# Kernel tuning notes

Measured on AMD Instinct MI355X. Metric: run time of the kernel, lower is better.

The kernel has to match this reference:

```python
import jax, jax.numpy as jnp
import numpy as np

H = 256; W = 256; TS = 4
EYE_Z = 2.732                     # nr camera position (0,0,2.732)
FOCAL = float(1.0 / np.tan(np.deg2rad(15.0)))  # 30-deg viewing angle
BIG = 1e10
EPS = 1e-8


def _render(vertices, faces, textures, angle):
    """Differentiable z-buffer rasterizer with trilinear per-face texture cubes.
    Ambient light = 1.0, directional = 0.0, so shading == sampled texture color."""
    v = vertices[0]                    # [V,3]
    f = faces[0]                       # [F,3] int
    tex = jnp.tanh(textures)[0]        # [F,TS,TS,TS,3]
    P = H * W

    # camera orbit: rotate mesh about y by angle (fraction of full turn)
    th = angle[0] * (2.0 * jnp.pi)
    c, s = jnp.cos(th), jnp.sin(th)
    x, y, z = v[:, 0], v[:, 1], v[:, 2]
    xr = c * x + s * z
    zr = -s * x + c * z
    depth = EYE_Z - zr                 # camera at (0,0,EYE_Z) looking down -z
    px = FOCAL * xr / depth
    py = FOCAL * y / depth

    fx = px[f]; fy = py[f]; fd = depth[f]      # [F,3]
    ax, bx, cx = fx[:, 0], fx[:, 1], fx[:, 2]
    ay, by, cy = fy[:, 0], fy[:, 1], fy[:, 2]

    # pixel centers in NDC [-1,1]
    xs = (jnp.arange(W) + 0.5) / W * 2.0 - 1.0
    ys = 1.0 - (jnp.arange(H) + 0.5) / H * 2.0
    gy, gx = jnp.meshgrid(ys, xs, indexing='ij')
    pxp = gx.reshape(-1)[:, None]      # [P,1]
    pyp = gy.reshape(-1)[:, None]

    area = (bx - ax) * (cy - ay) - (by - ay) * (cx - ax)
    valid = jnp.abs(area) > EPS
    denom = jnp.where(valid, area, 1.0)

    def edge(x0, y0, x1, y1):
        # normalized edge function -> barycentric weight, shape [P,F]
        return ((x1 - x0) * (pyp - y0) - (y1 - y0) * (pxp - x0)) / denom

    w0 = edge(bx, by, cx, cy)
    w1 = edge(cx, cy, ax, ay)
    w2 = 1.0 - w0 - w1
    inside = (w0 >= 0) & (w1 >= 0) & (w2 >= 0) & valid[None, :]

    zpix = w0 * fd[:, 0] + w1 * fd[:, 1] + w2 * fd[:, 2]   # interpolated depth
    zbuf = jnp.where(inside & (zpix > EPS), zpix, BIG)
    fidx = jnp.argmin(zbuf, axis=1)                        # [P] winning face
    hit = jnp.take_along_axis(zbuf, fidx[:, None], 1)[:, 0] < 0.5 * BIG

    w0s = jnp.take_along_axis(w0, fidx[:, None], 1)[:, 0]
    w1s = jnp.take_along_axis(w1, fidx[:, None], 1)[:, 0]
    pw = jnp.stack([w0s, w1s, 1.0 - w0s - w1s], axis=-1)   # [P,3] barycentric

    # trilinear sample of the per-face TSxTSxTS texture cube at barycentric coords
    u = jnp.clip(pw, 0.0, 1.0) * (TS - 1)
    i0 = jnp.clip(jnp.floor(u), 0, TS - 2).astype(jnp.int32)
    fr = u - i0
    texp = tex[fidx].reshape(P, TS * TS * TS, 3)           # [P,64,3]
    col = jnp.zeros((P, 3), dtype=textures.dtype)
    for a in (0, 1):
        for b in (0, 1):
            for cc in (0, 1):
                idxf = (i0[:, 0] + a) * TS * TS + (i0[:, 1] + b) * TS + (i0[:, 2] + cc)
                wc = (jnp.where(a, fr[:, 0], 1.0 - fr[:, 0])
                      * jnp.where(b, fr[:, 1], 1.0 - fr[:, 1])
                      * jnp.where(cc, fr[:, 2], 1.0 - fr[:, 2]))
                col = col + wc[:, None] * jnp.take_along_axis(texp, idxf[:, None, None], axis=1)[:, 0, :]
    col = jnp.where(hit[:, None], col, 0.0)                # black background
    return col.T.reshape(1, 3, H, W)


def setup_inputs():
    key = jax.random.key(0)
    k1, k2, k3, k4, k5 = jax.random.split(key, 5)
    V, F = 322, 640
    vertices = 0.4 * jax.random.normal(k1, (1, V, 3), dtype=jnp.float32)
    faces = jax.random.randint(k2, (1, F, 3), 0, V, dtype=jnp.int32)
    textures = 0.5 * jax.random.normal(k3, (1, F, TS, TS, TS, 3), dtype=jnp.float32)
    image_ref = jax.random.uniform(k4, (1, 3, H, W), dtype=jnp.float32)
    angle = jax.random.uniform(k5, (1,), dtype=jnp.float32)
    return {"vertices": vertices, "faces": faces, "textures": textures,
            "image_ref": image_ref, "angle": angle}


def reference(vertices, faces, textures, image_ref, angle):
    image = _render(vertices, faces, textures, angle)
    return jnp.sum((image - image_ref) ** 2)
```

## Files before the change

kernel.cpp:

```cpp
#include <hip/hip_runtime.h>
#include <math.h>

#define NH 256
#define NW 256
#define NP (NH*NW)
#define NF 640
#define NBLK 512
#define EYE_Z 2.732f
#define BIGF 1.0e10f
#define EPSF 1.0e-8f
#define FOCALF 3.7320508075688776f


__global__ __launch_bounds__(256, 2) void fused_kernel(
    const float* __restrict__ vertices,
    const int* __restrict__ faces,
    const float* __restrict__ textures,
    const float* __restrict__ angle,
    const float* __restrict__ ref,
    float* __restrict__ partials)
{
    __shared__ float4 sf[NF * 3];
    __shared__ float candZ[4][128];
    __shared__ int   candF[4][128];
    __shared__ float psum[2];

    int tid = threadIdx.x;
    int wave = tid >> 6;
    int lane = tid & 63;

    float th = angle[0] * 6.283185307179586f;
    float cth = cosf(th), sth = sinf(th);
    for (int j = tid; j < NF; j += 256) {
        float vx[3], vy[3], vd[3];
#pragma unroll
        for (int k = 0; k < 3; k++) {
            int vi = faces[j * 3 + k];
            float x = vertices[vi * 3 + 0];
            float y = vertices[vi * 3 + 1];
            float z = vertices[vi * 3 + 2];
            float xr = cth * x + sth * z;
            float zr = -sth * x + cth * z;
            float depth = EYE_Z - zr;
            vx[k] = FOCALF * xr / depth;
            vy[k] = FOCALF * y / depth;
            vd[k] = depth;
        }
        float ax = vx[0], ay = vy[0], bx = vx[1], by = vy[1], cx = vx[2], cy = vy[2];
        float area = (bx - ax) * (cy - ay) - (by - ay) * (cx - ax);
        float4 d0, d1, d2;
        if (fabsf(area) > EPSF) {
            float inv = 1.0f / area;
            float A0 = -(cy - by) * inv;
            float B0 = (cx - bx) * inv;
            float C0 = (bx * (cy - by) - by * (cx - bx)) * inv;
            float A1 = -(ay - cy) * inv;
            float B1 = (ax - cx) * inv;
            float C1 = (cx * (ay - cy) - cy * (ax - cx)) * inv;
            float zA = vd[0] - vd[2];
            float zB = vd[1] - vd[2];
            float Az = zA * A0 + zB * A1;
            float Bz = zA * B0 + zB * B1;
            float Cz = zA * C0 + zB * C1 + vd[2];
            d0 = make_float4(A0, B0, C0, A1);
            d1 = make_float4(B1, C1, Az, Bz);
            d2 = make_float4(Cz, 0.f, 0.f, 0.f);
        } else {
            d0 = make_float4(0.f, 0.f, -1.f, 0.f);
            d1 = make_float4(0.f, 0.f, 0.f, 0.f);
            d2 = make_float4(0.f, 0.f, 0.f, 0.f);
        }
        sf[j * 3 + 0] = d0;
        sf[j * 3 + 1] = d1;
        sf[j * 3 + 2] = d2;
    }
    __syncthreads();

    int base = blockIdx.x * 128;
    int row = base >> 8;
    int col0 = (base & 255) + lane;
    float px0 = ((float)col0 + 0.5f) * (1.0f / 128.0f) - 1.0f;
    float py = 1.0f - ((float)row + 0.5f) * (1.0f / 128.0f);

    float zmin0 = BIGF, zmin1 = BIGF;
    int best0 = wave * 160, best1 = wave * 160;
    int fbeg = wave * 160;
#pragma unroll 4
    for (int k = 0; k < 160; ++k) {
        int f = fbeg + k;
        float4 d0 = sf[f * 3 + 0];
        float4 d1 = sf[f * 3 + 1];
        float zC = sf[f * 3 + 2].x;
        float w0a = fmaf(d0.x, px0, fmaf(d0.y, py, d0.z));
        float w1a = fmaf(d0.w, px0, fmaf(d1.x, py, d1.y));
        float za  = fmaf(d1.z, px0, fmaf(d1.w, py, zC));
        float w0b = fmaf(0.5f, d0.x, w0a);
        float w1b = fmaf(0.5f, d0.w, w1a);
        float zb  = fmaf(0.5f, d1.z, za);
        float w2a = 1.f - w0a - w1a;
        float w2b = 1.f - w0b - w1b;
        float mna = fminf(fminf(w0a, w1a), w2a);
        float mnb = fminf(fminf(w0b, w1b), w2b);
        bool oka = (mna >= 0.f) && (za > EPSF) && (za < zmin0);
        bool okb = (mnb >= 0.f) && (zb > EPSF) && (zb < zmin1);
        zmin0 = oka ? za : zmin0;
        best0 = oka ? f : best0;
        zmin1 = okb ? zb : zmin1;
        best1 = okb ? f : best1;
    }
    candZ[wave][lane] = zmin0;
    candZ[wave][64 + lane] = zmin1;
    candF[wave][lane] = best0;
    candF[wave][64 + lane] = best1;
    __syncthreads();

    if (wave < 2) {
        int q = wave * 64 + lane;
        float zb = candZ[0][q];
        int fb = candF[0][q];
#pragma unroll
        for (int k = 1; k < 4; ++k) {
            float zk = candZ[k][q];
            int fk = candF[k][q];
            bool t = zk < zb;
            zb = t ? zk : zb;
            fb = t ? fk : fb;
        }
        bool hit = zb < 0.5f * BIGF;

        int p = base + q;
        float pxq = ((float)((base & 255) + q) + 0.5f) * (1.0f / 128.0f) - 1.0f;
        float4 d0 = sf[fb * 3 + 0];
        float4 d1 = sf[fb * 3 + 1];
        float bw0 = fmaf(d0.x, pxq, fmaf(d0.y, py, d0.z));
        float bw1 = fmaf(d0.w, pxq, fmaf(d1.x, py, d1.y));
        float pw2 = 1.f - bw0 - bw1;
        float u0 = fminf(fmaxf(bw0, 0.f), 1.f) * 3.f;
        float u1 = fminf(fmaxf(bw1, 0.f), 1.f) * 3.f;
        float u2 = fminf(fmaxf(pw2, 0.f), 1.f) * 3.f;
        int i0 = min(max((int)floorf(u0), 0), 2);
        int i1 = min(max((int)floorf(u1), 0), 2);
        int i2 = min(max((int)floorf(u2), 0), 2);
        float fr0 = u0 - (float)i0;
        float fr1 = u1 - (float)i1;
        float fr2 = u2 - (float)i2;

        const float* tb = textures + fb * 192;
        float cr = 0.f, cg = 0.f, cb = 0.f;
#pragma unroll
        for (int a = 0; a < 2; a++) {
#pragma unroll
            for (int bbi = 0; bbi < 2; bbi++) {
#pragma unroll
                for (int cc = 0; cc < 2; cc++) {
                    int idx = ((i0 + a) * 16 + (i1 + bbi) * 4 + (i2 + cc)) * 3;
                    float w = (a ? fr0 : 1.f - fr0) * (bbi ? fr1 : 1.f - fr1) * (cc ? fr2 : 1.f - fr2);
                    cr = fmaf(w, tanhf(tb[idx + 0]), cr);
                    cg = fmaf(w, tanhf(tb[idx + 1]), cg);
                    cb = fmaf(w, tanhf(tb[idx + 2]), cb);
                }
            }
        }
        if (!hit) { cr = 0.f; cg = 0.f; cb = 0.f; }

        float e0 = cr - ref[p];
        float e1 = cg - ref[NP + p];
        float e2 = cb - ref[2 * NP + p];
        float e = fmaf(e0, e0, fmaf(e1, e1, e2 * e2));
#pragma unroll
        for (int off = 32; off > 0; off >>= 1) e += __shfl_down(e, off, 64);
        if (lane == 0) psum[wave] = e;
    }
    __syncthreads();
    if (tid == 0) partials[blockIdx.x] = psum[0] + psum[1];
}

__global__ __launch_bounds__(256) void reduce_kernel(
    const float* __restrict__ partials, float* __restrict__ out)
{
    __shared__ float wsum[4];
    int tid = threadIdx.x;
    float s = partials[tid] + partials[tid + 256];
#pragma unroll
    for (int off = 32; off > 0; off >>= 1) s += __shfl_down(s, off, 64);
    int lane = tid & 63;
    int wid = tid >> 6;
    if (lane == 0) wsum[wid] = s;
    __syncthreads();
    if (tid == 0) out[0] = wsum[0] + wsum[1] + wsum[2] + wsum[3];
}

extern "C" void kernel_launch(void* const* d_in, const int* in_sizes, int n_in,
                              void* d_out, int out_size, void* d_ws, size_t ws_size,
                              hipStream_t stream) {
    const float* vertices = (const float*)d_in[0];
    const int* faces = (const int*)d_in[1];
    const float* textures = (const float*)d_in[2];
    const float* image_ref = (const float*)d_in[3];
    const float* angle = (const float*)d_in[4];
    float* out = (float*)d_out;
    float* partials = (float*)d_ws;

    fused_kernel<<<NBLK, 256, 0, stream>>>(vertices, faces, textures, angle,
                                           image_ref, partials);
    reduce_kernel<<<1, 256, 0, stream>>>(partials, out);
}
```

Baseline: 86.60 us.

## Tile-based face culling per block with compacted face lists and pretransformed textures

Each block now covers a 16x8 pixel tile and builds a compacted list of only the faces whose bounding box and edge functions overlap the tile, using ballot/popcount stream compaction in shared memory. The per-pixel depth test then loops over the culled list instead of all 640 faces. Vertices are projected once into shared memory instead of once per face corner. A separate prep kernel applies tanh to the textures once and pads them into float4 entries so each texel is fetched with one vector load. The change adds an extra kernel launch and several block barriers. The reduced face count per tile depends on the triangle sizes in the mesh.

Measured after the change: 75.67 us. 12.6% less time.

```diff
diff --git a/kernel.cpp b/kernel.cpp
--- a/kernel.cpp
+++ b/kernel.cpp
@@ -4,23 +4,43 @@
 #define NH 256
 #define NW 256
 #define NP (NH*NW)
+#define NV 322
 #define NF 640
-#define NBLK 512
 #define EYE_Z 2.732f
 #define BIGF 1.0e10f
 #define EPSF 1.0e-8f
 #define FOCALF 3.7320508075688776f
-
+#define TILE_W 16
+#define TILE_H 8
+#define NTX (NW/TILE_W)
+#define NTY (NH/TILE_H)
+#define NBLK (NTX*NTY)
+#define CULL_PAD 1e-5f
+
+
+__global__ void texprep_kernel(const float* __restrict__ textures,
+                               float4* __restrict__ texPad)
+{
+    int e = blockIdx.x * 256 + threadIdx.x;
+    float v = tanhf(textures[e]);
+    int fidx = e / 192;
+    int r = e - fidx * 192;
+    int t = r / 3;
+    int ch = r - t * 3;
+    ((float*)&texPad[fidx * 64 + t])[ch] = v;
+}
 
 __global__ __launch_bounds__(256, 2) void fused_kernel(
     const float* __restrict__ vertices,
     const int* __restrict__ faces,
-    const float* __restrict__ textures,
     const float* __restrict__ angle,
+    const float4* __restrict__ texPad,
     const float* __restrict__ ref,
     float* __restrict__ partials)
 {
-    __shared__ float4 sf[NF * 3];
+    __shared__ float4 pv[NV];
+    __shared__ float4 list[NF * 3];
+    __shared__ int wcnt[4];
     __shared__ float candZ[4][128];
     __shared__ int   candF[4][128];
     __shared__ float psum[2];
@@ -31,109 +51,140 @@
 
     float th = angle[0] * 6.283185307179586f;
     float cth = cosf(th), sth = sinf(th);
-    for (int j = tid; j < NF; j += 256) {
-        float vx[3], vy[3], vd[3];
-#pragma unroll
-        for (int k = 0; k < 3; k++) {
-            int vi = faces[j * 3 + k];
-            float x = vertices[vi * 3 + 0];
-            float y = vertices[vi * 3 + 1];
-            float z = vertices[vi * 3 + 2];
-            float xr = cth * x + sth * z;
-            float zr = -sth * x + cth * z;
-            float depth = EYE_Z - zr;
-            vx[k] = FOCALF * xr / depth;
-            vy[k] = FOCALF * y / depth;
-            vd[k] = depth;
-        }
-        float ax = vx[0], ay = vy[0], bx = vx[1], by = vy[1], cx = vx[2], cy = vy[2];
-        float area = (bx - ax) * (cy - ay) - (by - ay) * (cx - ax);
-        float4 d0, d1, d2;
-        if (fabsf(area) > EPSF) {
-            float inv = 1.0f / area;
-            float A0 = -(cy - by) * inv;
-            float B0 = (cx - bx) * inv;
-            float C0 = (bx * (cy - by) - by * (cx - bx)) * inv;
-            float A1 = -(ay - cy) * inv;
-            float B1 = (ax - cx) * inv;
-            float C1 = (cx * (ay - cy) - cy * (ax - cx)) * inv;
-            float zA = vd[0] - vd[2];
-            float zB = vd[1] - vd[2];
-            float Az = zA * A0 + zB * A1;
-            float Bz = zA * B0 + zB * B1;
-            float Cz = zA * C0 + zB * C1 + vd[2];
-            d0 = make_float4(A0, B0, C0, A1);
-            d1 = make_float4(B1, C1, Az, Bz);
-            d2 = make_float4(Cz, 0.f, 0.f, 0.f);
-        } else {
-            d0 = make_float4(0.f, 0.f, -1.f, 0.f);
-            d1 = make_float4(0.f, 0.f, 0.f, 0.f);
-            d2 = make_float4(0.f, 0.f, 0.f, 0.f);
-        }
-        sf[j * 3 + 0] = d0;
-        sf[j * 3 + 1] = d1;
-        sf[j * 3 + 2] = d2;
-    }
-    __syncthreads();
-
-    int base = blockIdx.x * 128;
-    int row = base >> 8;
-    int col0 = (base & 255) + lane;
-    float px0 = ((float)col0 + 0.5f) * (1.0f / 128.0f) - 1.0f;
-    float py = 1.0f - ((float)row + 0.5f) * (1.0f / 128.0f);
+    for (int t = tid; t < NV; t += 256) {
+        float x = vertices[t * 3 + 0];
+        float y = vertices[t * 3 + 1];
+        float z = vertices[t * 3 + 2];
+        float xr = cth * x + sth * z;
+        float zr = -sth * x + cth * z;
+        float depth = EYE_Z - zr;
+        pv[t] = make_float4(FOCALF * xr / depth, FOCALF * y / depth, depth, 0.f);
+    }
+    __syncthreads();
+
+    int tc = blockIdx.x & (NTX - 1);
+    int tr = blockIdx.x >> 4;
+    float x0 = ((float)(tc * TILE_W) + 0.5f) * (1.f / 128.f) - 1.f;
+    float x1 = ((float)(tc * TILE_W + TILE_W - 1) + 0.5f) * (1.f / 128.f) - 1.f;
+    float y1 = 1.f - ((float)(tr * TILE_H) + 0.5f) * (1.f / 128.f);
+    float y0 = 1.f - ((float)(tr * TILE_H + TILE_H - 1) + 0.5f) * (1.f / 128.f);
+
+    int nfl = 0;
+    for (int rd = 0; rd < 3; ++rd) {
+        int f = rd * 256 + tid;
+        bool accept = false;
+        float4 e0, e1, e2;
+        if (f < NF) {
+            int i0 = faces[f * 3 + 0], i1 = faces[f * 3 + 1], i2 = faces[f * 3 + 2];
+            float4 pa = pv[i0], pb = pv[i1], pc = pv[i2];
+            float area = (pb.x - pa.x) * (pc.y - pa.y) - (pb.y - pa.y) * (pc.x - pa.x);
+            if (fabsf(area) > EPSF) {
+                float xmn = fminf(fminf(pa.x, pb.x), pc.x);
+                float xmx = fmaxf(fmaxf(pa.x, pb.x), pc.x);
+                float ymn = fminf(fminf(pa.y, pb.y), pc.y);
+                float ymx = fmaxf(fmaxf(pa.y, pb.y), pc.y);
+                if (xmx >= x0 - CULL_PAD && xmn <= x1 + CULL_PAD &&
+                    ymx >= y0 - CULL_PAD && ymn <= y1 + CULL_PAD) {
+                    float inv = 1.0f / area;
+                    float A0 = -(pc.y - pb.y) * inv;
+                    float B0 =  (pc.x - pb.x) * inv;
+                    float C0 =  (pb.x * (pc.y - pb.y) - pb.y * (pc.x - pb.x)) * inv;
+                    float A1 = -(pa.y - pc.y) * inv;
+                    float B1 =  (pa.x - pc.x) * inv;
+                    float C1 =  (pc.x * (pa.y - pc.y) - pc.y * (pa.x - pc.x)) * inv;
+                    float A2 = -(A0 + A1), B2 = -(B0 + B1), C2 = 1.f - C0 - C1;
+                    float m0 = C0 + fmaxf(A0 * x0, A0 * x1) + fmaxf(B0 * y0, B0 * y1);
+                    float m1 = C1 + fmaxf(A1 * x0, A1 * x1) + fmaxf(B1 * y0, B1 * y1);
+                    float m2 = C2 + fmaxf(A2 * x0, A2 * x1) + fmaxf(B2 * y0, B2 * y1);
+                    if (m0 >= -CULL_PAD && m1 >= -CULL_PAD && m2 >= -CULL_PAD) {
+                        accept = true;
+                        float zA = pa.z - pc.z, zB = pb.z - pc.z;
+                        float Az = zA * A0 + zB * A1;
+                        float Bz = zA * B0 + zB * B1;
+                        float Cz = zA * C0 + zB * C1 + pc.z;
+                        e0 = make_float4(A0, B0, C0, A1);
+                        e1 = make_float4(B1, C1, Az, Bz);
+                        e2 = make_float4(Cz, __int_as_float(f), 0.f, 0.f);
+                    }
+                }
+            }
+        }
+        unsigned long long m = __ballot(accept);
+        if (lane == 0) wcnt[wave] = (int)__popcll(m);
+        __syncthreads();
+        int base = nfl;
+        if (wave > 0) base += wcnt[0];
+        if (wave > 1) base += wcnt[1];
+        if (wave > 2) base += wcnt[2];
+        int pos = base + (int)__popcll(m & ((1ULL << lane) - 1ULL));
+        if (accept) {
+            list[pos * 3 + 0] = e0;
+            list[pos * 3 + 1] = e1;
+            list[pos * 3 + 2] = e2;
+        }
+        nfl += wcnt[0] + wcnt[1] + wcnt[2] + wcnt[3];
+        __syncthreads();
+    }
+
+    int nflu = __builtin_amdgcn_readfirstlane(nfl);
+    int c0 = (nflu * wave) >> 2;
+    int c1 = (nflu * (wave + 1)) >> 2;
+    int colp = tc * TILE_W + (lane & 15);
+    int rowp = tr * TILE_H + (lane >> 4);
+    float px  = ((float)colp + 0.5f) * (1.f / 128.f) - 1.f;
+    float pya = 1.f - ((float)rowp + 0.5f) * (1.f / 128.f);
+    const float DPY = -0.03125f;
 
     float zmin0 = BIGF, zmin1 = BIGF;
-    int best0 = wave * 160, best1 = wave * 160;
-    int fbeg = wave * 160;
-#pragma unroll 4
-    for (int k = 0; k < 160; ++k) {
-        int f = fbeg + k;
-        float4 d0 = sf[f * 3 + 0];
-        float4 d1 = sf[f * 3 + 1];
-        float zC = sf[f * 3 + 2].x;
-        float w0a = fmaf(d0.x, px0, fmaf(d0.y, py, d0.z));
-        float w1a = fmaf(d0.w, px0, fmaf(d1.x, py, d1.y));
-        float za  = fmaf(d1.z, px0, fmaf(d1.w, py, zC));
-        float w0b = fmaf(0.5f, d0.x, w0a);
-        float w1b = fmaf(0.5f, d0.w, w1a);
-        float zb  = fmaf(0.5f, d1.z, za);
-        float w2a = 1.f - w0a - w1a;
-        float w2b = 1.f - w0b - w1b;
-        float mna = fminf(fminf(w0a, w1a), w2a);
-        float mnb = fminf(fminf(w0b, w1b), w2b);
-        bool oka = (mna >= 0.f) && (za > EPSF) && (za < zmin0);
-        bool okb = (mnb >= 0.f) && (zb > EPSF) && (zb < zmin1);
-        zmin0 = oka ? za : zmin0;
-        best0 = oka ? f : best0;
-        zmin1 = okb ? zb : zmin1;
-        best1 = okb ? f : best1;
-    }
-    candZ[wave][lane] = zmin0;
-    candZ[wave][64 + lane] = zmin1;
-    candF[wave][lane] = best0;
-    candF[wave][64 + lane] = best1;
+    int best0 = 0, best1 = 0;
+    for (int i = c0; i < c1; ++i) {
+        float4 d0 = list[i * 3 + 0];
+        float4 d1 = list[i * 3 + 1];
+        float czv = list[i * 3 + 2].x;
+        float w0a = fmaf(d0.x, px, fmaf(d0.y, pya, d0.z));
+        float w1a = fmaf(d0.w, px, fmaf(d1.x, pya, d1.y));
+        float za  = fmaf(d1.z, px, fmaf(d1.w, pya, czv));
+        float w0b = fmaf(DPY, d0.y, w0a);
+        float w1b = fmaf(DPY, d1.x, w1a);
+        float zb  = fmaf(DPY, d1.w, za);
+        float mna = fminf(fminf(w0a, w1a), 1.f - w0a - w1a);
+        float mnb = fminf(fminf(w0b, w1b), 1.f - w0b - w1b);
+        bool oka = (mna >= 0.f) && (za < zmin0);
+        bool okb = (mnb >= 0.f) && (zb < zmin1);
+        zmin0 = oka ? za : zmin0;  best0 = oka ? i : best0;
+        zmin1 = okb ? zb : zmin1;  best1 = okb ? i : best1;
+    }
+    candZ[wave][lane] = zmin0;      candF[wave][lane] = best0;
+    candZ[wave][lane + 64] = zmin1; candF[wave][lane + 64] = best1;
     __syncthreads();
 
     if (wave < 2) {
-        int q = wave * 64 + lane;
-        float zb = candZ[0][q];
-        int fb = candF[0][q];
+        int sq = wave * 64 + lane;
+        float zb = candZ[0][sq];
+        int fb = candF[0][sq];
 #pragma unroll
         for (int k = 1; k < 4; ++k) {
-            float zk = candZ[k][q];
-            int fk = candF[k][q];
+            float zk = candZ[k][sq];
+            int fk = candF[k][sq];
             bool t = zk < zb;
             zb = t ? zk : zb;
             fb = t ? fk : fb;
         }
         bool hit = zb < 0.5f * BIGF;
 
-        int p = base + q;
-        float pxq = ((float)((base & 255) + q) + 0.5f) * (1.0f / 128.0f) - 1.0f;
-        float4 d0 = sf[fb * 3 + 0];
-        float4 d1 = sf[fb * 3 + 1];
-        float bw0 = fmaf(d0.x, pxq, fmaf(d0.y, py, d0.z));
-        float bw1 = fmaf(d0.w, pxq, fmaf(d1.x, py, d1.y));
+        int colq = tc * TILE_W + (sq & 15);
+        int rowq = tr * TILE_H + (sq >> 4);
+        int p = rowq * 256 + colq;
+        float pxq = ((float)colq + 0.5f) * (1.f / 128.f) - 1.f;
+        float pyq = 1.f - ((float)rowq + 0.5f) * (1.f / 128.f);
+
+        float4 d0 = list[fb * 3 + 0];
+        float4 d1 = list[fb * 3 + 1];
+        int forig = __float_as_int(list[fb * 3 + 2].y);
+        int ftex = hit ? forig : 0;
+
+        float bw0 = fmaf(d0.x, pxq, fmaf(d0.y, pyq, d0.z));
+        float bw1 = fmaf(d0.w, pxq, fmaf(d1.x, pyq, d1.y));
         float pw2 = 1.f - bw0 - bw1;
         float u0 = fminf(fmaxf(bw0, 0.f), 1.f) * 3.f;
         float u1 = fminf(fmaxf(bw1, 0.f), 1.f) * 3.f;
@@ -145,7 +196,7 @@
         float fr1 = u1 - (float)i1;
         float fr2 = u2 - (float)i2;
 
-        const float* tb = textures + fb * 192;
+        const float4* tb = texPad + ftex * 64;
         float cr = 0.f, cg = 0.f, cb = 0.f;
 #pragma unroll
         for (int a = 0; a < 2; a++) {
@@ -153,20 +204,21 @@
             for (int bbi = 0; bbi < 2; bbi++) {
 #pragma unroll
                 for (int cc = 0; cc < 2; cc++) {
-                    int idx = ((i0 + a) * 16 + (i1 + bbi) * 4 + (i2 + cc)) * 3;
+                    int idx = (i0 + a) * 16 + (i1 + bbi) * 4 + (i2 + cc);
                     float w = (a ? fr0 : 1.f - fr0) * (bbi ? fr1 : 1.f - fr1) * (cc ? fr2 : 1.f - fr2);
-                    cr = fmaf(w, tanhf(tb[idx + 0]), cr);
-                    cg = fmaf(w, tanhf(tb[idx + 1]), cg);
-                    cb = fmaf(w, tanhf(tb[idx + 2]), cb);
+                    float4 t = tb[idx];
+                    cr = fmaf(w, t.x, cr);
+                    cg = fmaf(w, t.y, cg);
+                    cb = fmaf(w, t.z, cb);
                 }
             }
         }
         if (!hit) { cr = 0.f; cg = 0.f; cb = 0.f; }
 
-        float e0 = cr - ref[p];
-        float e1 = cg - ref[NP + p];
-        float e2 = cb - ref[2 * NP + p];
-        float e = fmaf(e0, e0, fmaf(e1, e1, e2 * e2));
+        float e0v = cr - ref[p];
+        float e1v = cg - ref[NP + p];
+        float e2v = cb - ref[2 * NP + p];
+        float e = fmaf(e0v, e0v, fmaf(e1v, e1v, e2v * e2v));
 #pragma unroll
         for (int off = 32; off > 0; off >>= 1) e += __shfl_down(e, off, 64);
         if (lane == 0) psum[wave] = e;
@@ -199,9 +251,12 @@
     const float* image_ref = (const float*)d_in[3];
     const float* angle = (const float*)d_in[4];
     float* out = (float*)d_out;
-    float* partials = (float*)d_ws;
-
-    fused_kernel<<<NBLK, 256, 0, stream>>>(vertices, faces, textures, angle,
-                                           image_ref, partials);
+
+    float4* texPad = (float4*)d_ws;
+    float* partials = (float*)((char*)d_ws + 655360);
+
+    texprep_kernel<<<480, 256, 0, stream>>>(textures, texPad);
+    fused_kernel<<<NBLK, 256, 0, stream>>>(vertices, faces, angle,
+                                           texPad, image_ref, partials);
     reduce_kernel<<<1, 256, 0, stream>>>(partials, out);
 }
```
